# Optimization experiments

Measured on AMD Instinct MI355X. Metric: run time of the kernel, lower is better.

## Reference

```python
import jax, jax.numpy as jnp
import numpy as np

DIM = 64
K = 8
B_TAIL = 3.0
HID = 128
BATCH = 131072
MIN_BIN_WIDTH = 1e-3
MIN_BIN_HEIGHT = 1e-3
MIN_DERIVATIVE = 1e-3


def setup_inputs() -> dict:
    key = jax.random.key(0)
    ks = jax.random.split(key, 9)
    nin = DIM // 2
    nout = (3 * K - 1) * (DIM - DIM // 2)
    dims = [nin, HID, HID, HID, nout]
    d = {"x": jax.random.normal(ks[0], (BATCH, DIM), jnp.float32)}
    for i in range(4):
        d[f"W{i+1}"] = jax.random.normal(ks[1 + 2 * i], (dims[i], dims[i + 1]), jnp.float32) / jnp.sqrt(dims[i])
        d[f"b{i+1}"] = jax.random.normal(ks[2 + 2 * i], (dims[i + 1],), jnp.float32) * 0.01
    return d


def _gather(a, idx):
    # a: [..., K or K+1], idx: [...] int -> [...]
    return jnp.take_along_axis(a, idx[..., None], axis=-1)[..., 0]


def _mlp(x, W1, b1, W2, b2, W3, b3, W4, b4):
    h = jax.nn.elu(x @ W1 + b1)
    h = jax.nn.elu(h @ W2 + b2)
    h = jax.nn.elu(h @ W3 + b3)
    return h @ W4 + b4


def _unconstrained_rqs_fwd(inputs, uw, uh, ud, tail_bound):
    # inputs: [B, D2]; uw/uh: [B, D2, K]; ud: [B, D2, K-1]
    num_bins = uw.shape[-1]
    left = bottom = -tail_bound
    right = top = tail_bound

    inside = (inputs >= -tail_bound) & (inputs <= tail_bound)
    x = jnp.clip(inputs, -tail_bound, tail_bound)  # safe values for spline math

    # pad derivatives and pin boundary slopes so spline matches identity tails
    const = float(np.log(np.exp(1.0 - MIN_DERIVATIVE) - 1.0))
    ud = jnp.pad(ud, [(0, 0)] * (ud.ndim - 1) + [(1, 1)], constant_values=const)

    widths = jax.nn.softmax(uw, axis=-1)
    widths = MIN_BIN_WIDTH + (1.0 - MIN_BIN_WIDTH * num_bins) * widths
    cumwidths = jnp.cumsum(widths, axis=-1)
    cumwidths = jnp.pad(cumwidths, [(0, 0)] * (cumwidths.ndim - 1) + [(1, 0)])
    cumwidths = (right - left) * cumwidths + left
    cumwidths = cumwidths.at[..., 0].set(left).at[..., -1].set(right)
    widths = cumwidths[..., 1:] - cumwidths[..., :-1]

    derivatives = MIN_DERIVATIVE + jax.nn.softplus(ud)

    heights = jax.nn.softmax(uh, axis=-1)
    heights = MIN_BIN_HEIGHT + (1.0 - MIN_BIN_HEIGHT * num_bins) * heights
    cumheights = jnp.cumsum(heights, axis=-1)
    cumheights = jnp.pad(cumheights, [(0, 0)] * (cumheights.ndim - 1) + [(1, 0)])
    cumheights = (top - bottom) * cumheights + bottom
    cumheights = cumheights.at[..., 0].set(bottom).at[..., -1].set(top)
    heights = cumheights[..., 1:] - cumheights[..., :-1]

    # searchsorted: number of bin edges <= x, minus one (eps on last edge)
    cw = cumwidths.at[..., -1].add(1e-6)
    bin_idx = jnp.sum((x[..., None] >= cw).astype(jnp.int32), axis=-1) - 1
    bin_idx = jnp.clip(bin_idx, 0, num_bins - 1)

    in_cw = _gather(cumwidths, bin_idx)
    in_w = _gather(widths, bin_idx)
    in_ch = _gather(cumheights, bin_idx)
    in_h = _gather(heights, bin_idx)
    delta = heights / widths
    in_delta = _gather(delta, bin_idx)
    in_d = _gather(derivatives, bin_idx)
    in_d1 = _gather(derivatives[..., 1:], bin_idx)

    theta = (x - in_cw) / in_w
    t1mt = theta * (1.0 - theta)
    numerator = in_h * (in_delta * theta ** 2 + in_d * t1mt)
    denominator = in_delta + (in_d + in_d1 - 2.0 * in_delta) * t1mt
    spline_out = in_ch + numerator / denominator
    deriv_num = in_delta ** 2 * (in_d1 * theta ** 2 + 2.0 * in_delta * t1mt + in_d * (1.0 - theta) ** 2)
    spline_ld = jnp.log(deriv_num) - 2.0 * jnp.log(denominator)

    outputs = jnp.where(inside, spline_out, inputs)
    logabsdet = jnp.where(inside, spline_ld, 0.0)
    return outputs, logabsdet


def reference(x, W1, b1, W2, b2, W3, b3, W4, b4):
    d_half = DIM // 2
    x1, x2 = x[:, :d_half], x[:, d_half:]
    out = _mlp(x1, W1, b1, W2, b2, W3, b3, W4, b4)
    out = out.reshape(-1, DIM - d_half, 3 * K - 1)
    W = out[..., :K]
    H = out[..., K:2 * K]
    D = out[..., 2 * K:]
    y2, ld = _unconstrained_rqs_fwd(x2, W, H, D, B_TAIL)
    log_det = jnp.sum(ld, axis=1)
    return jnp.concatenate([x1, y2], axis=1), log_det
```

## Files before the change

### kernel.cpp

```cpp
#include <hip/hip_runtime.h>
#include <hip/hip_bf16.h>
#include <math.h>

typedef _Float16 f16_t;
typedef _Float16 f16x4 __attribute__((ext_vector_type(4)));
typedef _Float16 f16x8 __attribute__((ext_vector_type(8)));
typedef float f32x4 __attribute__((ext_vector_type(4)));

#define BATCH 131072
#define MTILE 64
#define NBLK (BATCH / MTILE)

#define W1F 0
#define W2F 4096
#define W3F 20480
#define W4F 36864

__global__ __launch_bounds__(256) void convert_weights_kernel(
    const float* __restrict__ W1, const float* __restrict__ W2,
    const float* __restrict__ W3, const float* __restrict__ W4,
    f16_t* __restrict__ wf) {
  int tid = blockIdx.x * 256 + threadIdx.x;
  if (tid >= 16896) return;
  int lane = tid & 63;
  int l16 = lane & 15, lhi = lane >> 4;
  const float* W; int ncols, col, k0; bool zero = false;
  if (tid < 512) {
    int n = tid >> 6;
    W = W1; ncols = 128; col = n * 16 + l16; k0 = lhi * 8;
  } else if (tid < 2560) {
    int g = tid - 512; int n = g >> 8, s = (g >> 6) & 3;
    W = W2; ncols = 128; col = n * 16 + l16; k0 = s * 32 + lhi * 8;
  } else if (tid < 4608) {
    int g = tid - 2560; int n = g >> 8, s = (g >> 6) & 3;
    W = W3; ncols = 128; col = n * 16 + l16; k0 = s * 32 + lhi * 8;
  } else {
    int g = tid - 4608; int t = g >> 8, s = (g >> 6) & 3;
    int c = t / 6, n = t - c * 6;
    int colc = n * 16 + l16;
    W = W4; ncols = 736; col = c * 92 + colc; k0 = s * 32 + lhi * 8;
    zero = (colc >= 92);
  }
  f16x8 v;
#pragma unroll
  for (int j = 0; j < 8; ++j)
    v[j] = zero ? (f16_t)0.f : (f16_t)W[(k0 + j) * ncols + col];
  *(f16x8*)(wf + (size_t)tid * 8) = v;
}

__device__ __forceinline__ float elu(float v) {
  return v > 0.f ? v : (__expf(v) - 1.f);
}

__device__ __forceinline__ void rqs_task(const f16_t* P, float xv,
                                         float& yout, float& ldout) {
  f16x8 pw = *(const f16x8*)P;
  f16x8 ph = *(const f16x8*)(P + 8);
  f16x8 pd = *(const f16x8*)(P + 16);

  float ew[8], sw = 0.f;
#pragma unroll
  for (int i = 0; i < 8; ++i) { ew[i] = __expf((float)pw[i]); sw += ew[i]; }
  float invw = 0.992f * __builtin_amdgcn_rcpf(sw);
  float cw[9]; cw[0] = -3.f;
  float accw = 0.f;
#pragma unroll
  for (int i = 0; i < 8; ++i) {
    accw += 0.001f + ew[i] * invw;
    cw[i + 1] = -3.f + 6.f * accw;
  }
  cw[8] = 3.f;
  float wd[8];
#pragma unroll
  for (int i = 0; i < 8; ++i) wd[i] = cw[i + 1] - cw[i];

  float eh[8], sh = 0.f;
#pragma unroll
  for (int i = 0; i < 8; ++i) { eh[i] = __expf((float)ph[i]); sh += eh[i]; }
  float invh = 0.992f * __builtin_amdgcn_rcpf(sh);
  float ch[9]; ch[0] = -3.f;
  float acch = 0.f;
#pragma unroll
  for (int i = 0; i < 8; ++i) {
    acch += 0.001f + eh[i] * invh;
    ch[i + 1] = -3.f + 6.f * acch;
  }
  ch[8] = 3.f;
  float ht[8];
#pragma unroll
  for (int i = 0; i < 8; ++i) ht[i] = ch[i + 1] - ch[i];

  float xc = fminf(fmaxf(xv, -3.f), 3.f);
  int bin = 0;
#pragma unroll
  for (int i = 1; i < 8; ++i) bin += (xc >= cw[i]) ? 1 : 0;

  float in_cw = cw[0], in_w = wd[0], in_ch = ch[0], in_h = ht[0];
  float sd  = (float)pd[0];
  float sd1 = (float)pd[0];
#pragma unroll
  for (int i = 1; i < 8; ++i) {
    bool g = (bin >= i);
    in_cw = g ? cw[i] : in_cw;  in_w = g ? wd[i] : in_w;
    in_ch = g ? ch[i] : in_ch;  in_h = g ? ht[i] : in_h;
    sd    = g ? (float)pd[i - 1] : sd;
  }
#pragma unroll
  for (int i = 1; i < 7; ++i)
    sd1 = (bin >= i) ? (float)pd[i] : sd1;

  float spd  = fmaxf(sd,  0.f) + __logf(1.f + __expf(-fabsf(sd)));
  float spd1 = fmaxf(sd1, 0.f) + __logf(1.f + __expf(-fabsf(sd1)));
  float in_d  = (bin == 0) ? 1.f : 0.001f + spd;
  float in_d1 = (bin == 7) ? 1.f : 0.001f + spd1;

  float rw = __builtin_amdgcn_rcpf(in_w);
  float dlt = in_h * rw;
  float th = (xc - in_cw) * rw;
  float om = 1.f - th;
  float t1 = th * om;
  float num = in_h * (dlt * th * th + in_d * t1);
  float den = dlt + (in_d + in_d1 - 2.f * dlt) * t1;
  float rden = __builtin_amdgcn_rcpf(den);
  float yo = in_ch + num * rden;
  float dn = dlt * dlt * (in_d1 * th * th + 2.f * dlt * t1 + in_d * om * om);
  float ldv = __logf(dn * rden * rden);
  bool inside = (xv >= -3.f) && (xv <= 3.f);
  yout = inside ? yo : xv;
  ldout = inside ? ldv : 0.f;
}

__device__ __forceinline__ void mid_layer_ip(f16_t* hH,
                                             const f16_t* __restrict__ wseg,
                                             const float* __restrict__ bg,
                                             int wv, int l16, int lhi, int lane) {
  f16x8 a[4];
#pragma unroll
  for (int s = 0; s < 4; ++s)
    a[s] = *(const f16x8*)&hH[(wv * 16 + l16) * 136 + s * 32 + lhi * 8];
#pragma unroll
  for (int n = 0; n < 8; ++n) {
    f32x4 acc = {0.f, 0.f, 0.f, 0.f};
#pragma unroll
    for (int s = 0; s < 4; ++s) {
      f16x8 b = *(const f16x8*)(wseg + (size_t)((n * 4 + s) * 64 + lane) * 8);
      acc = __builtin_amdgcn_mfma_f32_16x16x32_f16(a[s], b, acc, 0, 0, 0);
    }
    float bias = bg[n * 16 + l16];
#pragma unroll
    for (int r = 0; r < 4; ++r)
      hH[(wv * 16 + lhi * 4 + r) * 136 + n * 16 + l16] =
          (f16_t)elu(acc[r] + bias);
  }
}

__global__ __launch_bounds__(256, 4) void nsf_fused_kernel(
    const float* __restrict__ x,
    const float* __restrict__ b1g, const float* __restrict__ b2g,
    const float* __restrict__ b3g, const float* __restrict__ b4g,
    const f16_t* __restrict__ wf,
    float* __restrict__ out) {
  __shared__ f16_t hH[MTILE * 136];
  __shared__ f16_t prm[MTILE * 4 * 24];
  __shared__ float x2s[MTILE * 33];

  const int tid = threadIdx.x;
  const int lane = tid & 63;
  const int wv = tid >> 6;
  const int l16 = lane & 15, lhi = lane >> 4;
  const int row0 = blockIdx.x * MTILE;

  {
    const float4* x4 = (const float4*)(x + (size_t)row0 * 64);
    float4* o4 = (float4*)(out + (size_t)row0 * 64);
#pragma unroll
    for (int it = 0; it < 4; ++it) {
      int idx = tid + it * 256;
      int row = idx >> 4, q = idx & 15;
      float4 v = x4[row * 16 + q];
      if (q < 8) {
        o4[row * 16 + q] = v;
        f16x4 p = {(f16_t)v.x, (f16_t)v.y, (f16_t)v.z, (f16_t)v.w};
        *(f16x4*)&hH[row * 136 + q * 4] = p;
      } else {
        int cb = row * 33 + (q - 8) * 4;
        x2s[cb + 0] = v.x; x2s[cb + 1] = v.y;
        x2s[cb + 2] = v.z; x2s[cb + 3] = v.w;
      }
    }
  }
  __syncthreads();

  {
    f16x8 a = *(const f16x8*)&hH[(wv * 16 + l16) * 136 + lhi * 8];
#pragma unroll
    for (int n = 0; n < 8; ++n) {
      f16x8 b = *(const f16x8*)(wf + W1F + (size_t)(n * 64 + lane) * 8);
      f32x4 acc = {0.f, 0.f, 0.f, 0.f};
      acc = __builtin_amdgcn_mfma_f32_16x16x32_f16(a, b, acc, 0, 0, 0);
      float bias = b1g[n * 16 + l16];
#pragma unroll
      for (int r = 0; r < 4; ++r)
        hH[(wv * 16 + lhi * 4 + r) * 136 + n * 16 + l16] =
            (f16_t)elu(acc[r] + bias);
    }
  }
  __syncthreads();

  mid_layer_ip(hH, wf + W2F, b2g, wv, l16, lhi, lane);
  __syncthreads();
  mid_layer_ip(hH, wf + W3F, b3g, wv, l16, lhi, lane);
  __syncthreads();

  {
    f16x8 a4[4];
#pragma unroll
    for (int s = 0; s < 4; ++s)
      a4[s] = *(const f16x8*)&hH[(wv * 16 + l16) * 136 + s * 32 + lhi * 8];

    const int srow = tid >> 2;
    const int sjj = tid & 3;
    float ldp = 0.f;

    for (int c = 0; c < 8; ++c) {
#pragma unroll
      for (int n = 0; n < 6; ++n) {
        f32x4 acc = {0.f, 0.f, 0.f, 0.f};
#pragma unroll
        for (int s = 0; s < 4; ++s) {
          f16x8 b = *(const f16x8*)(wf + W4F +
                      (size_t)(((c * 6 + n) * 4 + s) * 64 + lane) * 8);
          acc = __builtin_amdgcn_mfma_f32_16x16x32_f16(a4[s], b, acc, 0, 0, 0);
        }
        int colc = n * 16 + l16;
        if (colc < 92) {
          int dm = (colc * 90) >> 11;
          int j = colc - dm * 23;
          float bias = b4g[c * 92 + colc];
#pragma unroll
          for (int r = 0; r < 4; ++r)
            prm[((wv * 16 + lhi * 4 + r) * 4 + dm) * 24 + j] =
                (f16_t)(acc[r] + bias);
        }
      }
      __syncthreads();

      {
        int jg = c * 4 + sjj;
        float xv = x2s[srow * 33 + jg];
        float y0, l0;
        rqs_task(prm + (srow * 4 + sjj) * 24, xv, y0, l0);
        out[(size_t)(row0 + srow) * 64 + 32 + jg] = y0;
        ldp += l0;
      }
      __syncthreads();
    }

    ldp += __shfl_xor(ldp, 1, 64);
    ldp += __shfl_xor(ldp, 2, 64);
    if ((tid & 3) == 0)
      out[(size_t)BATCH * 64 + row0 + srow] = ldp;
  }
}

extern "C" void kernel_launch(void* const* d_in, const int* in_sizes, int n_in,
                              void* d_out, int out_size, void* d_ws, size_t ws_size,
                              hipStream_t stream) {
  const float* x  = (const float*)d_in[0];
  const float* W1 = (const float*)d_in[1];
  const float* b1 = (const float*)d_in[2];
  const float* W2 = (const float*)d_in[3];
  const float* b2 = (const float*)d_in[4];
  const float* W3 = (const float*)d_in[5];
  const float* b3 = (const float*)d_in[6];
  const float* W4 = (const float*)d_in[7];
  const float* b4 = (const float*)d_in[8];
  f16_t* wf = (f16_t*)d_ws;
  float* out = (float*)d_out;

  hipLaunchKernelGGL(convert_weights_kernel, dim3(66), dim3(256), 0, stream,
                     W1, W2, W3, W4, wf);
  hipLaunchKernelGGL(nsf_fused_kernel, dim3(NBLK), dim3(256), 0, stream,
                     x, b1, b2, b3, b4, wf, out);
}
```

Before: 99.81 us.

## Double-buffer final layer params across prm and hH to halve barriers

The final layer's eight chunks are now processed in pairs. Even chunks write spline parameters into prm and odd chunks into the freed hH buffer, so one barrier per chunk can be removed. The layer-4 MFMA work for the next chunk can then overlap with the RQS evaluation of the previous one. An extra barrier after loading a4 keeps hH safe to reuse. Correctness depends on hH being large enough and on ordering across the prm and hH reuse.

```diff
diff --git a/kernel.cpp b/kernel.cpp
--- a/kernel.cpp
+++ b/kernel.cpp
@@ -217,26 +217,30 @@
 #pragma unroll
     for (int s = 0; s < 4; ++s)
       a4[s] = *(const f16x8*)&hH[(wv * 16 + l16) * 136 + s * 32 + lhi * 8];
+    __syncthreads();
 
     const int srow = tid >> 2;
     const int sjj = tid & 3;
     float ldp = 0.f;
 
-    for (int c = 0; c < 8; ++c) {
+#pragma unroll
+    for (int cp = 0; cp < 4; ++cp) {
+      const int cA = 2 * cp, cB = 2 * cp + 1;
+
 #pragma unroll
       for (int n = 0; n < 6; ++n) {
         f32x4 acc = {0.f, 0.f, 0.f, 0.f};
 #pragma unroll
         for (int s = 0; s < 4; ++s) {
           f16x8 b = *(const f16x8*)(wf + W4F +
-                      (size_t)(((c * 6 + n) * 4 + s) * 64 + lane) * 8);
+                      (size_t)(((cA * 6 + n) * 4 + s) * 64 + lane) * 8);
           acc = __builtin_amdgcn_mfma_f32_16x16x32_f16(a4[s], b, acc, 0, 0, 0);
         }
         int colc = n * 16 + l16;
         if (colc < 92) {
           int dm = (colc * 90) >> 11;
           int j = colc - dm * 23;
-          float bias = b4g[c * 92 + colc];
+          float bias = b4g[cA * 92 + colc];
 #pragma unroll
           for (int r = 0; r < 4; ++r)
             prm[((wv * 16 + lhi * 4 + r) * 4 + dm) * 24 + j] =
@@ -246,14 +250,43 @@
       __syncthreads();
 
       {
-        int jg = c * 4 + sjj;
+        int jg = cA * 4 + sjj;
         float xv = x2s[srow * 33 + jg];
         float y0, l0;
         rqs_task(prm + (srow * 4 + sjj) * 24, xv, y0, l0);
         out[(size_t)(row0 + srow) * 64 + 32 + jg] = y0;
         ldp += l0;
       }
+#pragma unroll
+      for (int n = 0; n < 6; ++n) {
+        f32x4 acc = {0.f, 0.f, 0.f, 0.f};
+#pragma unroll
+        for (int s = 0; s < 4; ++s) {
+          f16x8 b = *(const f16x8*)(wf + W4F +
+                      (size_t)(((cB * 6 + n) * 4 + s) * 64 + lane) * 8);
+          acc = __builtin_amdgcn_mfma_f32_16x16x32_f16(a4[s], b, acc, 0, 0, 0);
+        }
+        int colc = n * 16 + l16;
+        if (colc < 92) {
+          int dm = (colc * 90) >> 11;
+          int j = colc - dm * 23;
+          float bias = b4g[cB * 92 + colc];
+#pragma unroll
+          for (int r = 0; r < 4; ++r)
+            hH[((wv * 16 + lhi * 4 + r) * 4 + dm) * 24 + j] =
+                (f16_t)(acc[r] + bias);
+        }
+      }
       __syncthreads();
+
+      {
+        int jg = cB * 4 + sjj;
+        float xv = x2s[srow * 33 + jg];
+        float y0, l0;
+        rqs_task(hH + (srow * 4 + sjj) * 24, xv, y0, l0);
+        out[(size_t)(row0 + srow) * 64 + 32 + jg] = y0;
+        ldp += l0;
+      }
     }
 
     ldp += __shfl_xor(ldp, 1, 64);
```

New measurement: 117.4 us. +17.6%, slower.

## Software-pipeline final GEMM chunks with RQS and fold log2e into W4 for exp2

Applied to the files above, without the earlier changes.

Restructures the last-layer loop so the MFMA work for chunk c+1 is issued before the spline evaluation of chunk c, with the results held in registers and stored to shared memory afterwards. The goal is to overlap matrix-core work with the transcendental-heavy spline math. The weight-conversion kernel now prescales the width and height logits of W4 and b4 by log2(e), so the spline can call exp2f directly. It also computes bin widths and heights from the selected softmax term instead of from cumulative differences. The trade-offs are more registers for the six live accumulators, an extra barrier per chunk, and slight fp16 rounding differences from the prescaling.

```diff
diff --git a/kernel.cpp b/kernel.cpp
--- a/kernel.cpp
+++ b/kernel.cpp
@@ -10,21 +10,31 @@
 #define BATCH 131072
 #define MTILE 64
 #define NBLK (BATCH / MTILE)
+#define LOG2E 1.4426950408889634f
 
 #define W1F 0
 #define W2F 4096
 #define W3F 20480
 #define W4F 36864
+#define B4S_OFF 67584
 
 __global__ __launch_bounds__(256) void convert_weights_kernel(
     const float* __restrict__ W1, const float* __restrict__ W2,
     const float* __restrict__ W3, const float* __restrict__ W4,
-    f16_t* __restrict__ wf) {
+    const float* __restrict__ b4, f16_t* __restrict__ wf,
+    float* __restrict__ b4s) {
   int tid = blockIdx.x * 256 + threadIdx.x;
-  if (tid >= 16896) return;
+  if (tid >= 16896) {
+    int i = tid - 16896;
+    if (i < 736) {
+      float s = ((i % 23) < 16) ? LOG2E : 1.f;
+      b4s[i] = b4[i] * s;
+    }
+    return;
+  }
   int lane = tid & 63;
   int l16 = lane & 15, lhi = lane >> 4;
-  const float* W; int ncols, col, k0; bool zero = false;
+  const float* W; int ncols, col, k0; bool zero = false; float scale = 1.f;
   if (tid < 512) {
     int n = tid >> 6;
     W = W1; ncols = 128; col = n * 16 + l16; k0 = lhi * 8;
@@ -40,11 +50,12 @@
     int colc = n * 16 + l16;
     W = W4; ncols = 736; col = c * 92 + colc; k0 = s * 32 + lhi * 8;
     zero = (colc >= 92);
+    if (!zero) scale = ((col % 23) < 16) ? LOG2E : 1.f;
   }
   f16x8 v;
 #pragma unroll
   for (int j = 0; j < 8; ++j)
-    v[j] = zero ? (f16_t)0.f : (f16_t)W[(k0 + j) * ncols + col];
+    v[j] = zero ? (f16_t)0.f : (f16_t)(W[(k0 + j) * ncols + col] * scale);
   *(f16x8*)(wf + (size_t)tid * 8) = v;
 }
 
@@ -60,54 +71,50 @@
 
   float ew[8], sw = 0.f;
 #pragma unroll
-  for (int i = 0; i < 8; ++i) { ew[i] = __expf((float)pw[i]); sw += ew[i]; }
+  for (int i = 0; i < 8; ++i) { ew[i] = exp2f((float)pw[i]); sw += ew[i]; }
   float invw = 0.992f * __builtin_amdgcn_rcpf(sw);
-  float cw[9]; cw[0] = -3.f;
+  float cw[8]; cw[0] = -3.f;
   float accw = 0.f;
 #pragma unroll
-  for (int i = 0; i < 8; ++i) {
+  for (int i = 0; i < 7; ++i) {
     accw += 0.001f + ew[i] * invw;
     cw[i + 1] = -3.f + 6.f * accw;
   }
-  cw[8] = 3.f;
-  float wd[8];
-#pragma unroll
-  for (int i = 0; i < 8; ++i) wd[i] = cw[i + 1] - cw[i];
 
   float eh[8], sh = 0.f;
 #pragma unroll
-  for (int i = 0; i < 8; ++i) { eh[i] = __expf((float)ph[i]); sh += eh[i]; }
+  for (int i = 0; i < 8; ++i) { eh[i] = exp2f((float)ph[i]); sh += eh[i]; }
   float invh = 0.992f * __builtin_amdgcn_rcpf(sh);
-  float ch[9]; ch[0] = -3.f;
+  float ch[8]; ch[0] = -3.f;
   float acch = 0.f;
 #pragma unroll
-  for (int i = 0; i < 8; ++i) {
+  for (int i = 0; i < 7; ++i) {
     acch += 0.001f + eh[i] * invh;
     ch[i + 1] = -3.f + 6.f * acch;
   }
-  ch[8] = 3.f;
-  float ht[8];
-#pragma unroll
-  for (int i = 0; i < 8; ++i) ht[i] = ch[i + 1] - ch[i];
 
   float xc = fminf(fmaxf(xv, -3.f), 3.f);
   int bin = 0;
 #pragma unroll
   for (int i = 1; i < 8; ++i) bin += (xc >= cw[i]) ? 1 : 0;
 
-  float in_cw = cw[0], in_w = wd[0], in_ch = ch[0], in_h = ht[0];
+  float in_cw = cw[0], in_ch = ch[0];
+  float ewsel = ew[0], ehsel = eh[0];
   float sd  = (float)pd[0];
   float sd1 = (float)pd[0];
 #pragma unroll
   for (int i = 1; i < 8; ++i) {
     bool g = (bin >= i);
-    in_cw = g ? cw[i] : in_cw;  in_w = g ? wd[i] : in_w;
-    in_ch = g ? ch[i] : in_ch;  in_h = g ? ht[i] : in_h;
+    in_cw = g ? cw[i] : in_cw;  in_ch = g ? ch[i] : in_ch;
+    ewsel = g ? ew[i] : ewsel;  ehsel = g ? eh[i] : ehsel;
     sd    = g ? (float)pd[i - 1] : sd;
   }
 #pragma unroll
   for (int i = 1; i < 7; ++i)
     sd1 = (bin >= i) ? (float)pd[i] : sd1;
+
+  float in_w = fmaf(ewsel * invw, 6.f, 0.006f);
+  float in_h = fmaf(ehsel * invh, 6.f, 0.006f);
 
   float spd  = fmaxf(sd,  0.f) + __logf(1.f + __expf(-fabsf(sd)));
   float spd1 = fmaxf(sd1, 0.f) + __logf(1.f + __expf(-fabsf(sd1)));
@@ -154,10 +161,42 @@
   }
 }
 
+__device__ __forceinline__ void gemm4_chunk(const f16_t* __restrict__ wf4,
+                                            const f16x8 a4[4], int lane,
+                                            f32x4 acc[6]) {
+#pragma unroll
+  for (int n = 0; n < 6; ++n) {
+    acc[n] = {0.f, 0.f, 0.f, 0.f};
+#pragma unroll
+    for (int s = 0; s < 4; ++s) {
+      f16x8 b = *(const f16x8*)(wf4 + (size_t)((n * 4 + s) * 64 + lane) * 8);
+      acc[n] = __builtin_amdgcn_mfma_f32_16x16x32_f16(a4[s], b, acc[n], 0, 0, 0);
+    }
+  }
+}
+
+__device__ __forceinline__ void store_chunk(f16_t* prm, const f32x4 acc[6],
+                                            const float* __restrict__ b4s,
+                                            int c, int wv, int l16, int lhi) {
+#pragma unroll
+  for (int n = 0; n < 6; ++n) {
+    int colc = n * 16 + l16;
+    if (colc < 92) {
+      int dm = (colc * 90) >> 11;
+      int j = colc - dm * 23;
+      float bias = b4s[c * 92 + colc];
+#pragma unroll
+      for (int r = 0; r < 4; ++r)
+        prm[((wv * 16 + lhi * 4 + r) * 4 + dm) * 24 + j] =
+            (f16_t)(acc[n][r] + bias);
+    }
+  }
+}
+
 __global__ __launch_bounds__(256, 4) void nsf_fused_kernel(
     const float* __restrict__ x,
     const float* __restrict__ b1g, const float* __restrict__ b2g,
-    const float* __restrict__ b3g, const float* __restrict__ b4g,
+    const float* __restrict__ b3g, const float* __restrict__ b4s,
     const f16_t* __restrict__ wf,
     float* __restrict__ out) {
   __shared__ f16_t hH[MTILE * 136];
@@ -221,29 +260,16 @@
     const int srow = tid >> 2;
     const int sjj = tid & 3;
     float ldp = 0.f;
-
+    f32x4 accn[6];
+
+    gemm4_chunk(wf + W4F, a4, lane, accn);
+    store_chunk(prm, accn, b4s, 0, wv, l16, lhi);
+    __syncthreads();
+
+#pragma unroll
     for (int c = 0; c < 8; ++c) {
-#pragma unroll
-      for (int n = 0; n < 6; ++n) {
-        f32x4 acc = {0.f, 0.f, 0.f, 0.f};
-#pragma unroll
-        for (int s = 0; s < 4; ++s) {
-          f16x8 b = *(const f16x8*)(wf + W4F +
-                      (size_t)(((c * 6 + n) * 4 + s) * 64 + lane) * 8);
-          acc = __builtin_amdgcn_mfma_f32_16x16x32_f16(a4[s], b, acc, 0, 0, 0);
-        }
-        int colc = n * 16 + l16;
-        if (colc < 92) {
-          int dm = (colc * 90) >> 11;
-          int j = colc - dm * 23;
-          float bias = b4g[c * 92 + colc];
-#pragma unroll
-          for (int r = 0; r < 4; ++r)
-            prm[((wv * 16 + lhi * 4 + r) * 4 + dm) * 24 + j] =
-                (f16_t)(acc[r] + bias);
-        }
-      }
-      __syncthreads();
+      if (c < 7)
+        gemm4_chunk(wf + W4F + (size_t)(c + 1) * 6 * 4 * 64 * 8, a4, lane, accn);
 
       {
         int jg = c * 4 + sjj;
@@ -254,6 +280,11 @@
         ldp += l0;
       }
       __syncthreads();
+
+      if (c < 7) {
+        store_chunk(prm, accn, b4s, c + 1, wv, l16, lhi);
+        __syncthreads();
+      }
     }
 
     ldp += __shfl_xor(ldp, 1, 64);
@@ -276,10 +307,11 @@
   const float* W4 = (const float*)d_in[7];
   const float* b4 = (const float*)d_in[8];
   f16_t* wf = (f16_t*)d_ws;
+  float* b4s = (float*)d_ws + B4S_OFF;
   float* out = (float*)d_out;
 
-  hipLaunchKernelGGL(convert_weights_kernel, dim3(66), dim3(256), 0, stream,
-                     W1, W2, W3, W4, wf);
+  hipLaunchKernelGGL(convert_weights_kernel, dim3(69), dim3(256), 0, stream,
+                     W1, W2, W3, W4, b4, wf, b4s);
   hipLaunchKernelGGL(nsf_fused_kernel, dim3(NBLK), dim3(256), 0, stream,
-                     x, b1, b2, b3, b4, wf, out);
-}
+                     x, b1, b2, b3, b4s, wf, out);
+}
```

Measured after the change: 111.4 us. 11.6% more time.
